# Optimization experiments

Hardware: AMD Instinct MI355X
Metric: run time of the kernel (lower is better)

Reference implementation:

```python
import jax, jax.numpy as jnp
import numpy as np

B, L, D = 4096, 50, 128
N_ITEMS, N_CATS, N_RATINGS = 100000, 1000, 5


def setup_inputs() -> dict:
    key = jax.random.key(0)
    ks = jax.random.split(key, 16)
    s = 0.05
    inp = {
        "nodes": jax.random.randint(ks[0], (B,), 0, N_ITEMS),
        "history_vc": jax.random.randint(ks[1], (B, L), 0, N_CATS),
        "history_r": jax.random.randint(ks[2], (B, L), 0, N_RATINGS),
        # embedding tables (c2e=categories, v2e=items, r2e=ratings)
        "c2e": jax.random.normal(ks[3], (N_CATS, D), jnp.float32) * s,
        "v2e": jax.random.normal(ks[4], (N_ITEMS, D), jnp.float32) * s,
        "r2e": jax.random.normal(ks[5], (N_RATINGS, D), jnp.float32) * s,
        # w_r1: Linear(2D, D); w_r2: Linear(D, D)
        "w_r1_w": jax.random.normal(ks[6], (D, 2 * D), jnp.float32) * s,
        "w_r1_b": jnp.zeros((D,), jnp.float32),
        "w_r2_w": jax.random.normal(ks[7], (D, D), jnp.float32) * s,
        "w_r2_b": jnp.zeros((D,), jnp.float32),
        # GraphRec Attention: att1 Linear(2D,D), att2 Linear(D,D), att3 Linear(D,1)
        "att1_w": jax.random.normal(ks[8], (D, 2 * D), jnp.float32) * s,
        "att1_b": jnp.zeros((D,), jnp.float32),
        "att2_w": jax.random.normal(ks[9], (D, D), jnp.float32) * s,
        "att2_b": jnp.zeros((D,), jnp.float32),
        "att3_w": jax.random.normal(ks[10], (1, D), jnp.float32) * s,
        "att3_b": jnp.zeros((1,), jnp.float32),
    }
    return inp


def reference(nodes, history_vc, history_r, c2e, v2e, r2e,
              w_r1_w, w_r1_b, w_r2_w, w_r2_b,
              att1_w, att1_b, att2_w, att2_b, att3_w, att3_b):
    # vc=True: neighbor histories index the category table, nodes index items
    e_vc = c2e[history_vc]          # [B, L, D]
    e_r = r2e[history_r]            # [B, L, D]
    vc_rep = v2e[nodes]             # [B, D]

    x = jnp.concatenate([e_vc, e_r], axis=-1)                      # [B, L, 2D]
    x = jax.nn.relu(jnp.einsum('blk,dk->bld', x, w_r1_w) + w_r1_b)
    o_history = jax.nn.relu(jnp.einsum('blk,dk->bld', x, w_r2_w) + w_r2_b)  # [B, L, D]

    # Attention: cat(o_history, node rep repeated) -> 2-layer relu MLP -> scalar -> softmax over L
    u = jnp.broadcast_to(vc_rep[:, None, :], o_history.shape)      # [B, L, D]
    a = jnp.concatenate([o_history, u], axis=-1)                   # [B, L, 2D]
    a = jax.nn.relu(jnp.einsum('blk,dk->bld', a, att1_w) + att1_b)
    a = jax.nn.relu(jnp.einsum('blk,dk->bld', a, att2_w) + att2_b)
    logits = jnp.einsum('bld,od->blo', a, att3_w)[..., 0] + att3_b[0]  # [B, L]
    att_w = jax.nn.softmax(logits, axis=1)                         # [B, L]

    # weighted sum over neighbors: o_history.T @ att_w per node
    to_feats = jnp.einsum('bl,bld->bd', att_w, o_history)          # [B, D]
    return to_feats
```

## Files before the change

kernel.cpp:

```cpp
#include <hip/hip_runtime.h>


#define NB 8
#define NTHR 512

#define WS_W1 0
#define WS_W2 4096
#define WS_A1 6144
#define WS_A2 10240
#define WS_FRAGS 12288

typedef __attribute__((ext_vector_type(8))) short short8;
typedef __attribute__((ext_vector_type(4))) float f32x4;

__device__ __forceinline__ float relu_f(float x) { return x > 0.f ? x : 0.f; }

__device__ __forceinline__ short f2bf(float f) {
  union { float f; unsigned u; } v; v.f = f;
  unsigned r = v.u + 0x7FFFu + ((v.u >> 16) & 1u);
  return (short)(r >> 16);
}

__device__ __forceinline__ float bf2f(short s) {
  union { unsigned u; float f; } v; v.u = ((unsigned)(unsigned short)s) << 16;
  return v.f;
}

__device__ __forceinline__ short8 cvt8(float4 a, float4 b) {
  short8 r;
  r[0] = f2bf(a.x); r[1] = f2bf(a.y); r[2] = f2bf(a.z); r[3] = f2bf(a.w);
  r[4] = f2bf(b.x); r[5] = f2bf(b.y); r[6] = f2bf(b.z); r[7] = f2bf(b.w);
  return r;
}

__device__ __forceinline__ short8 wfrag(const float* __restrict__ W, int ldk,
                                        int d, int k) {
  const float4* p = (const float4*)(W + (size_t)d * ldk + k);
  return cvt8(p[0], p[1]);
}

__global__ __launch_bounds__(256)
void conv_weights(const float* __restrict__ w1, const float* __restrict__ w2,
                  const float* __restrict__ a1w, const float* __restrict__ a2w,
                  short* __restrict__ ws) {
  const int id = blockIdx.x * 256 + threadIdx.x;
  const float* W; int ldk, base;
  if (id < WS_W2)      { W = w1;  ldk = 256; base = WS_W1; }
  else if (id < WS_A1) { W = w2;  ldk = 128; base = WS_W2; }
  else if (id < WS_A2) { W = a1w; ldk = 256; base = WS_A1; }
  else                 { W = a2w; ldk = 128; base = WS_A2; }
  const int local = id - base;
  const int col = local & 127, kg = (local >> 7) & 3, s = local >> 9;
  const float4* p = (const float4*)(W + (size_t)col * ldk + s * 32 + kg * 8);
  *(short8*)(ws + (size_t)id * 8) = cvt8(p[0], p[1]);
}

template <int NS, int ROWB>
__device__ __forceinline__ void run_phase(const char* __restrict__ Abase,
                                          const short8* wf, f32x4 acc[4],
                                          int r16, int kg) {
#pragma unroll
  for (int mt = 0; mt < 4; ++mt) acc[mt] = (f32x4){0.f, 0.f, 0.f, 0.f};
#pragma unroll
  for (int s = 0; s < NS; ++s) {
    const int kb = s * 64 + kg * 16;
#pragma unroll
    for (int mt = 0; mt < 4; ++mt) {
      const int row = mt * 16 + r16;
      short8 a = *(const short8*)(Abase + row * ROWB + (kb ^ ((row & 7) << 4)));
      acc[mt] = __builtin_amdgcn_mfma_f32_16x16x32_bf16(a, wf[s], acc[mt], 0, 0, 0);
    }
  }
}

__global__ __launch_bounds__(NTHR, 2)
void vc_agg_kernel(const int* __restrict__ nodes,
                   const int* __restrict__ hvc,
                   const int* __restrict__ hr,
                   const float* __restrict__ c2e,
                   const float* __restrict__ v2e,
                   const float* __restrict__ r2e,
                   const float* __restrict__ w1, const float* __restrict__ b1,
                   const float* __restrict__ w2, const float* __restrict__ b2,
                   const float* __restrict__ a1w, const float* __restrict__ a1b,
                   const float* __restrict__ a2w, const float* __restrict__ a2b,
                   const float* __restrict__ a3w,
                   const short* __restrict__ wsf, int usePre,
                   float* __restrict__ out)
{
  __shared__ __align__(16) char sA3[64 * 512];
  __shared__ __align__(16) char sX[64 * 256];
  __shared__ float sU[128];
  __shared__ int sIvc[50], sIr[50];
  __shared__ float sPlog[8 * 64];
  __shared__ float sWts[64];
  __shared__ float sPs[4 * 128];

  const int tid = threadIdx.x;
  const int w = tid >> 6;
  const int lane = tid & 63;
  const int r16 = lane & 15;
  const int kg = lane >> 4;
  const int col = w * 16 + r16;

  const float b1v = b1[col], b2v = b2[col];
  const float a1bv = a1b[col], a2bv = a2b[col], a3v = a3w[col];

  const int el = tid >> 3, esub = tid & 7;

  for (int ib = 0; ib < NB; ++ib) {
    const int b = blockIdx.x * NB + ib;

    if (tid < 50) { sIvc[tid] = hvc[b * 50 + tid]; sIr[tid] = hr[b * 50 + tid]; }
    if (tid < 128) sU[tid] = v2e[(size_t)nodes[b] * 128 + tid];
    __syncthreads();

    if (el < 50) {
      const int kk = esub * 32;
      const float* src = (kk < 128) ? (c2e + (size_t)sIvc[el] * 128 + kk)
                                    : (r2e + (size_t)sIr[el] * 128 + (kk - 128));
#pragma unroll
      for (int j = 0; j < 4; ++j) {
        const float4* p = (const float4*)(src + j * 8);
        const int kb = (kk + j * 8) * 2;
        *(short8*)(sA3 + el * 512 + (kb ^ ((el & 7) << 4))) = cvt8(p[0], p[1]);
      }
    }
    __syncthreads();

    f32x4 acc[4];

    {
      short8 wf[8];
      if (usePre) {
#pragma unroll
        for (int s = 0; s < 8; ++s)
          wf[s] = *(const short8*)(wsf + (size_t)(WS_W1 + (s * 4 + kg) * 128 + col) * 8);
      } else {
#pragma unroll
        for (int s = 0; s < 8; ++s) wf[s] = wfrag(w1, 256, col, s * 32 + kg * 8);
      }
      run_phase<8, 512>(sA3, wf, acc, r16, kg);
    }
#pragma unroll
    for (int mt = 0; mt < 4; ++mt)
#pragma unroll
      for (int r = 0; r < 4; ++r) {
        const int row = mt * 16 + kg * 4 + r;
        *(short*)(sX + row * 256 + ((col * 2) ^ ((row & 7) << 4))) =
            f2bf(relu_f(acc[mt][r] + b1v));
      }
    __syncthreads();

    {
      short8 wf[4];
      if (usePre) {
#pragma unroll
        for (int s = 0; s < 4; ++s)
          wf[s] = *(const short8*)(wsf + (size_t)(WS_W2 + (s * 4 + kg) * 128 + col) * 8);
      } else {
#pragma unroll
        for (int s = 0; s < 4; ++s) wf[s] = wfrag(w2, 128, col, s * 32 + kg * 8);
      }
      run_phase<4, 256>(sX, wf, acc, r16, kg);
    }
#pragma unroll
    for (int mt = 0; mt < 4; ++mt)
#pragma unroll
      for (int r = 0; r < 4; ++r) {
        const int row = mt * 16 + kg * 4 + r;
        *(short*)(sA3 + row * 512 + ((col * 2) ^ ((row & 7) << 4))) =
            f2bf(relu_f(acc[mt][r] + b2v));
      }
    {
      const float* up = sU + esub * 16;
#pragma unroll
      for (int m = 0; m < 2; ++m) {
        const int kb = (128 + esub * 16 + m * 8) * 2;
        *(short8*)(sA3 + el * 512 + (kb ^ ((el & 7) << 4))) =
            cvt8(*(const float4*)(up + m * 8), *(const float4*)(up + m * 8 + 4));
      }
    }
    __syncthreads();

    {
      short8 wf[8];
      if (usePre) {
#pragma unroll
        for (int s = 0; s < 8; ++s)
          wf[s] = *(const short8*)(wsf + (size_t)(WS_A1 + (s * 4 + kg) * 128 + col) * 8);
      } else {
#pragma unroll
        for (int s = 0; s < 8; ++s) wf[s] = wfrag(a1w, 256, col, s * 32 + kg * 8);
      }
      run_phase<8, 512>(sA3, wf, acc, r16, kg);
    }
#pragma unroll
    for (int mt = 0; mt < 4; ++mt)
#pragma unroll
      for (int r = 0; r < 4; ++r) {
        const int row = mt * 16 + kg * 4 + r;
        *(short*)(sX + row * 256 + ((col * 2) ^ ((row & 7) << 4))) =
            f2bf(relu_f(acc[mt][r] + a1bv));
      }
    __syncthreads();

    {
      short8 wf[4];
      if (usePre) {
#pragma unroll
        for (int s = 0; s < 4; ++s)
          wf[s] = *(const short8*)(wsf + (size_t)(WS_A2 + (s * 4 + kg) * 128 + col) * 8);
      } else {
#pragma unroll
        for (int s = 0; s < 4; ++s) wf[s] = wfrag(a2w, 128, col, s * 32 + kg * 8);
      }
      run_phase<4, 256>(sX, wf, acc, r16, kg);
    }
    {
      float pm[4][4];
#pragma unroll
      for (int mt = 0; mt < 4; ++mt)
#pragma unroll
        for (int r = 0; r < 4; ++r) {
          float v = relu_f(acc[mt][r] + a2bv) * a3v;
#pragma unroll
          for (int off = 1; off < 16; off <<= 1) v += __shfl_xor(v, off);
          pm[mt][r] = v;
        }
      if (r16 == 0) {
#pragma unroll
        for (int mt = 0; mt < 4; ++mt)
#pragma unroll
          for (int r = 0; r < 4; ++r)
            sPlog[w * 64 + mt * 16 + kg * 4 + r] = pm[mt][r];
      }
    }
    __syncthreads();

    if (tid < 64) {
      float s = 0.f;
#pragma unroll
      for (int ww = 0; ww < 8; ++ww) s += sPlog[ww * 64 + tid];
      float x = (tid < 50) ? s : -3.4e38f;
#pragma unroll
      for (int off = 32; off; off >>= 1) x = fmaxf(x, __shfl_xor(x, off));
      const float e = (tid < 50) ? __expf(s - x) : 0.f;
      float t = e;
#pragma unroll
      for (int off = 32; off; off >>= 1) t += __shfl_xor(t, off);
      if (tid < 50) sWts[tid] = e / t;
    }
    __syncthreads();

    {
      const int d = tid & 127, g = tid >> 7;
      const int lb = g * 13, le = (lb + 13 < 50) ? lb + 13 : 50;
      float s = 0.f;
      for (int l = lb; l < le; ++l) {
        const short ov = *(const short*)(sA3 + l * 512 + ((d * 2) ^ ((l & 7) << 4)));
        s = fmaf(sWts[l], bf2f(ov), s);
      }
      sPs[g * 128 + d] = s;
    }
    __syncthreads();
    if (tid < 128)
      out[(size_t)b * 128 + tid] =
          sPs[tid] + sPs[128 + tid] + sPs[256 + tid] + sPs[384 + tid];
    __syncthreads();
  }
}

extern "C" void kernel_launch(void* const* d_in, const int* in_sizes, int n_in,
                              void* d_out, int out_size, void* d_ws, size_t ws_size,
                              hipStream_t stream) {
  const int* nodes = (const int*)d_in[0];
  const int* hvc   = (const int*)d_in[1];
  const int* hr    = (const int*)d_in[2];
  const float* c2e = (const float*)d_in[3];
  const float* v2e = (const float*)d_in[4];
  const float* r2e = (const float*)d_in[5];
  const float* w1  = (const float*)d_in[6];
  const float* b1  = (const float*)d_in[7];
  const float* w2  = (const float*)d_in[8];
  const float* b2  = (const float*)d_in[9];
  const float* a1w = (const float*)d_in[10];
  const float* a1b = (const float*)d_in[11];
  const float* a2w = (const float*)d_in[12];
  const float* a2b = (const float*)d_in[13];
  const float* a3w = (const float*)d_in[14];
  float* out = (float*)d_out;

  const int usePre = (ws_size >= (size_t)WS_FRAGS * 16) ? 1 : 0;
  short* wsf = (short*)d_ws;
  if (usePre)
    conv_weights<<<WS_FRAGS / 256, 256, 0, stream>>>(w1, w2, a1w, a2w, wsf);

  vc_agg_kernel<<<4096 / NB, NTHR, 0, stream>>>(nodes, hvc, hr, c2e, v2e, r2e,
                                                w1, b1, w2, b2, a1w, a1b, a2w,
                                                a2b, a3w, wsf, usePre, out);
}
```

Before: 278.6 us.

## Halve block size and compute two column tiles per wave to reuse A fragments

Shrinks the block from 8 to 4 waves and has each wave compute two 16-column output tiles. One A fragment loaded from shared memory now feeds two MFMAs, halving LDS reads per MFMA. Weight fragments are loaded per k-step instead of being held in a register array, and each block handles 4 batch rows instead of 8, giving more blocks. The costs are more accumulator registers per thread and fewer waves per block, which could lower occupancy and latency hiding.

```diff
diff --git a/kernel.cpp b/kernel.cpp
--- a/kernel.cpp
+++ b/kernel.cpp
@@ -1,8 +1,8 @@
 #include <hip/hip_runtime.h>
 
 
-#define NB 8
-#define NTHR 512
+#define NB 4
+#define NTHR 256
 
 #define WS_W1 0
 #define WS_W2 4096
@@ -56,19 +56,35 @@
 }
 
 template <int NS, int ROWB>
-__device__ __forceinline__ void run_phase(const char* __restrict__ Abase,
-                                          const short8* wf, f32x4 acc[4],
-                                          int r16, int kg) {
-#pragma unroll
-  for (int mt = 0; mt < 4; ++mt) acc[mt] = (f32x4){0.f, 0.f, 0.f, 0.f};
+__device__ __forceinline__ void run_phase2(const char* __restrict__ Abase,
+                                           const short* __restrict__ wsf,
+                                           int wsBase,
+                                           const float* __restrict__ Wfb,
+                                           int ldk, int usePre,
+                                           f32x4 acc[2][4], int r16, int kg,
+                                           int col0) {
+#pragma unroll
+  for (int nt = 0; nt < 2; ++nt)
+#pragma unroll
+    for (int mt = 0; mt < 4; ++mt) acc[nt][mt] = (f32x4){0.f, 0.f, 0.f, 0.f};
 #pragma unroll
   for (int s = 0; s < NS; ++s) {
+    short8 wfa, wfb;
+    if (usePre) {
+      const size_t base = (size_t)(wsBase + (s * 4 + kg) * 128 + col0) * 8;
+      wfa = *(const short8*)(wsf + base);
+      wfb = *(const short8*)(wsf + base + 128);
+    } else {
+      wfa = wfrag(Wfb, ldk, col0, s * 32 + kg * 8);
+      wfb = wfrag(Wfb, ldk, col0 + 16, s * 32 + kg * 8);
+    }
     const int kb = s * 64 + kg * 16;
 #pragma unroll
     for (int mt = 0; mt < 4; ++mt) {
       const int row = mt * 16 + r16;
       short8 a = *(const short8*)(Abase + row * ROWB + (kb ^ ((row & 7) << 4)));
-      acc[mt] = __builtin_amdgcn_mfma_f32_16x16x32_bf16(a, wf[s], acc[mt], 0, 0, 0);
+      acc[0][mt] = __builtin_amdgcn_mfma_f32_16x16x32_bf16(a, wfa, acc[0][mt], 0, 0, 0);
+      acc[1][mt] = __builtin_amdgcn_mfma_f32_16x16x32_bf16(a, wfb, acc[1][mt], 0, 0, 0);
     }
   }
 }
@@ -92,21 +108,24 @@
   __shared__ __align__(16) char sX[64 * 256];
   __shared__ float sU[128];
   __shared__ int sIvc[50], sIr[50];
-  __shared__ float sPlog[8 * 64];
+  __shared__ float sPlog[4 * 64];
   __shared__ float sWts[64];
-  __shared__ float sPs[4 * 128];
+  __shared__ float sPs[2 * 128];
 
   const int tid = threadIdx.x;
   const int w = tid >> 6;
   const int lane = tid & 63;
   const int r16 = lane & 15;
   const int kg = lane >> 4;
-  const int col = w * 16 + r16;
-
-  const float b1v = b1[col], b2v = b2[col];
-  const float a1bv = a1b[col], a2bv = a2b[col], a3v = a3w[col];
-
-  const int el = tid >> 3, esub = tid & 7;
+  const int col0 = w * 32 + r16;
+
+  const float b1v0 = b1[col0],  b1v1 = b1[col0 + 16];
+  const float b2v0 = b2[col0],  b2v1 = b2[col0 + 16];
+  const float a1b0 = a1b[col0], a1b1 = a1b[col0 + 16];
+  const float a2b0 = a2b[col0], a2b1 = a2b[col0 + 16];
+  const float a3v0 = a3w[col0], a3v1 = a3w[col0 + 16];
+
+  const int el = tid >> 2, esub = tid & 3;
 
   for (int ib = 0; ib < NB; ++ib) {
     const int b = blockIdx.x * NB + ib;
@@ -116,11 +135,11 @@
     __syncthreads();
 
     if (el < 50) {
-      const int kk = esub * 32;
+      const int kk = esub * 64;
       const float* src = (kk < 128) ? (c2e + (size_t)sIvc[el] * 128 + kk)
                                     : (r2e + (size_t)sIr[el] * 128 + (kk - 128));
 #pragma unroll
-      for (int j = 0; j < 4; ++j) {
+      for (int j = 0; j < 8; ++j) {
         const float4* p = (const float4*)(src + j * 8);
         const int kb = (kk + j * 8) * 2;
         *(short8*)(sA3 + el * 512 + (kb ^ ((el & 7) << 4))) = cvt8(p[0], p[1]);
@@ -128,112 +147,84 @@
     }
     __syncthreads();
 
-    f32x4 acc[4];
-
+    f32x4 acc[2][4];
+
+    run_phase2<8, 512>(sA3, wsf, WS_W1, w1, 256, usePre, acc, r16, kg, col0);
+#pragma unroll
+    for (int nt = 0; nt < 2; ++nt) {
+      const float bb = nt ? b1v1 : b1v0;
+      const int c = col0 + nt * 16;
+#pragma unroll
+      for (int mt = 0; mt < 4; ++mt)
+#pragma unroll
+        for (int r = 0; r < 4; ++r) {
+          const int row = mt * 16 + kg * 4 + r;
+          *(short*)(sX + row * 256 + ((c * 2) ^ ((row & 7) << 4))) =
+              f2bf(relu_f(acc[nt][mt][r] + bb));
+        }
+    }
+    __syncthreads();
+
+    run_phase2<4, 256>(sX, wsf, WS_W2, w2, 128, usePre, acc, r16, kg, col0);
+#pragma unroll
+    for (int nt = 0; nt < 2; ++nt) {
+      const float bb = nt ? b2v1 : b2v0;
+      const int c = col0 + nt * 16;
+#pragma unroll
+      for (int mt = 0; mt < 4; ++mt)
+#pragma unroll
+        for (int r = 0; r < 4; ++r) {
+          const int row = mt * 16 + kg * 4 + r;
+          *(short*)(sA3 + row * 512 + ((c * 2) ^ ((row & 7) << 4))) =
+              f2bf(relu_f(acc[nt][mt][r] + bb));
+        }
+    }
     {
-      short8 wf[8];
-      if (usePre) {
-#pragma unroll
-        for (int s = 0; s < 8; ++s)
-          wf[s] = *(const short8*)(wsf + (size_t)(WS_W1 + (s * 4 + kg) * 128 + col) * 8);
-      } else {
-#pragma unroll
-        for (int s = 0; s < 8; ++s) wf[s] = wfrag(w1, 256, col, s * 32 + kg * 8);
-      }
-      run_phase<8, 512>(sA3, wf, acc, r16, kg);
-    }
-#pragma unroll
-    for (int mt = 0; mt < 4; ++mt)
-#pragma unroll
-      for (int r = 0; r < 4; ++r) {
-        const int row = mt * 16 + kg * 4 + r;
-        *(short*)(sX + row * 256 + ((col * 2) ^ ((row & 7) << 4))) =
-            f2bf(relu_f(acc[mt][r] + b1v));
-      }
-    __syncthreads();
-
-    {
-      short8 wf[4];
-      if (usePre) {
-#pragma unroll
-        for (int s = 0; s < 4; ++s)
-          wf[s] = *(const short8*)(wsf + (size_t)(WS_W2 + (s * 4 + kg) * 128 + col) * 8);
-      } else {
-#pragma unroll
-        for (int s = 0; s < 4; ++s) wf[s] = wfrag(w2, 128, col, s * 32 + kg * 8);
-      }
-      run_phase<4, 256>(sX, wf, acc, r16, kg);
-    }
-#pragma unroll
-    for (int mt = 0; mt < 4; ++mt)
-#pragma unroll
-      for (int r = 0; r < 4; ++r) {
-        const int row = mt * 16 + kg * 4 + r;
-        *(short*)(sA3 + row * 512 + ((col * 2) ^ ((row & 7) << 4))) =
-            f2bf(relu_f(acc[mt][r] + b2v));
-      }
-    {
-      const float* up = sU + esub * 16;
-#pragma unroll
-      for (int m = 0; m < 2; ++m) {
-        const int kb = (128 + esub * 16 + m * 8) * 2;
+      const float* up = sU + esub * 32;
+#pragma unroll
+      for (int m = 0; m < 4; ++m) {
+        const int kb = (128 + esub * 32 + m * 8) * 2;
         *(short8*)(sA3 + el * 512 + (kb ^ ((el & 7) << 4))) =
             cvt8(*(const float4*)(up + m * 8), *(const float4*)(up + m * 8 + 4));
       }
     }
     __syncthreads();
 
+    run_phase2<8, 512>(sA3, wsf, WS_A1, a1w, 256, usePre, acc, r16, kg, col0);
+#pragma unroll
+    for (int nt = 0; nt < 2; ++nt) {
+      const float bb = nt ? a1b1 : a1b0;
+      const int c = col0 + nt * 16;
+#pragma unroll
+      for (int mt = 0; mt < 4; ++mt)
+#pragma unroll
+        for (int r = 0; r < 4; ++r) {
+          const int row = mt * 16 + kg * 4 + r;
+          *(short*)(sX + row * 256 + ((c * 2) ^ ((row & 7) << 4))) =
+              f2bf(relu_f(acc[nt][mt][r] + a1b0 * 0.f + bb));
+        }
+    }
+    __syncthreads();
+
+    run_phase2<4, 256>(sX, wsf, WS_A2, a2w, 128, usePre, acc, r16, kg, col0);
     {
-      short8 wf[8];
-      if (usePre) {
-#pragma unroll
-        for (int s = 0; s < 8; ++s)
-          wf[s] = *(const short8*)(wsf + (size_t)(WS_A1 + (s * 4 + kg) * 128 + col) * 8);
-      } else {
-#pragma unroll
-        for (int s = 0; s < 8; ++s) wf[s] = wfrag(a1w, 256, col, s * 32 + kg * 8);
-      }
-      run_phase<8, 512>(sA3, wf, acc, r16, kg);
-    }
-#pragma unroll
-    for (int mt = 0; mt < 4; ++mt)
-#pragma unroll
-      for (int r = 0; r < 4; ++r) {
-        const int row = mt * 16 + kg * 4 + r;
-        *(short*)(sX + row * 256 + ((col * 2) ^ ((row & 7) << 4))) =
-            f2bf(relu_f(acc[mt][r] + a1bv));
-      }
-    __syncthreads();
-
-    {
-      short8 wf[4];
-      if (usePre) {
-#pragma unroll
-        for (int s = 0; s < 4; ++s)
-          wf[s] = *(const short8*)(wsf + (size_t)(WS_A2 + (s * 4 + kg) * 128 + col) * 8);
-      } else {
-#pragma unroll
-        for (int s = 0; s < 4; ++s) wf[s] = wfrag(a2w, 128, col, s * 32 + kg * 8);
-      }
-      run_phase<4, 256>(sX, wf, acc, r16, kg);
-    }
-    {
-      float pm[4][4];
-#pragma unroll
-      for (int mt = 0; mt < 4; ++mt)
-#pragma unroll
-        for (int r = 0; r < 4; ++r) {
-          float v = relu_f(acc[mt][r] + a2bv) * a3v;
+#pragma unroll
+      for (int mt = 0; mt < 4; ++mt) {
+        float pv[4];
+#pragma unroll
+        for (int r = 0; r < 4; ++r) {
+          float v0 = relu_f(acc[0][mt][r] + a2b0) * a3v0;
+          float v1 = relu_f(acc[1][mt][r] + a2b1) * a3v1;
+          float v = v0 + v1;
 #pragma unroll
           for (int off = 1; off < 16; off <<= 1) v += __shfl_xor(v, off);
-          pm[mt][r] = v;
-        }
-      if (r16 == 0) {
-#pragma unroll
-        for (int mt = 0; mt < 4; ++mt)
+          pv[r] = v;
+        }
+        if (r16 == 0) {
 #pragma unroll
           for (int r = 0; r < 4; ++r)
-            sPlog[w * 64 + mt * 16 + kg * 4 + r] = pm[mt][r];
+            sPlog[w * 64 + mt * 16 + kg * 4 + r] = pv[r];
+        }
       }
     }
     __syncthreads();
@@ -241,7 +232,7 @@
     if (tid < 64) {
       float s = 0.f;
 #pragma unroll
-      for (int ww = 0; ww < 8; ++ww) s += sPlog[ww * 64 + tid];
+      for (int ww = 0; ww < 4; ++ww) s += sPlog[ww * 64 + tid];
       float x = (tid < 50) ? s : -3.4e38f;
 #pragma unroll
       for (int off = 32; off; off >>= 1) x = fmaxf(x, __shfl_xor(x, off));
@@ -255,7 +246,7 @@
 
     {
       const int d = tid & 127, g = tid >> 7;
-      const int lb = g * 13, le = (lb + 13 < 50) ? lb + 13 : 50;
+      const int lb = g * 25, le = lb + 25;
       float s = 0.f;
       for (int l = lb; l < le; ++l) {
         const short ov = *(const short*)(sA3 + l * 512 + ((d * 2) ^ ((l & 7) << 4)));
@@ -265,8 +256,7 @@
     }
     __syncthreads();
     if (tid < 128)
-      out[(size_t)b * 128 + tid] =
-          sPs[tid] + sPs[128 + tid] + sPs[256 + tid] + sPs[384 + tid];
+      out[(size_t)b * 128 + tid] = sPs[tid] + sPs[128 + tid];
     __syncthreads();
   }
 }
```

After: 359.2 us. 1.29x slower.
